# Optimization experiments

Measured on AMD Instinct MI355X. Metric: run time of the kernel, lower is better.

## Reference

```python
import jax, jax.numpy as jnp
import numpy as np
from jax import lax

N = 100000      # nodes
F_IN = 128      # dataset.num_features
H = 64          # hidden
E = 1600000     # edges
G = 1000        # graphs (equal-sized, contiguous)
PER = N // G    # nodes per graph = 100
K = 30          # sort-pool k
KS = 3          # conv1d kernel = num_layers


def setup_inputs() -> dict:
    key = jax.random.key(0)
    ks = jax.random.split(key, 20)
    lin = lambda k, i, o: (jax.random.normal(k, (i, o), jnp.float32) / np.sqrt(i)).astype(jnp.float32)
    return {
        "x": jax.random.normal(ks[0], (N, F_IN), jnp.float32),
        "src": jax.random.randint(ks[1], (E,), 0, N, dtype=jnp.int32),
        "dst": jax.random.randint(ks[2], (E,), 0, N, dtype=jnp.int32),
        "num_graphs": G,
        # SAGEConv 1: lin_l (aggr, with bias), lin_r (self, no bias)
        "wl1": lin(ks[3], F_IN, H), "wr1": lin(ks[4], F_IN, H), "b1": jnp.zeros((H,), jnp.float32),
        "wl2": lin(ks[5], H, H), "wr2": lin(ks[6], H, H), "b2": jnp.zeros((H,), jnp.float32),
        "wl3": lin(ks[7], H, H), "wr3": lin(ks[8], H, H), "b3": jnp.zeros((H,), jnp.float32),
        # Conv1d(hidden=64 -> 32, kernel=3): weight [O, I, K]
        "cw": (jax.random.normal(ks[9], (32, H, KS), jnp.float32) / np.sqrt(H * KS)).astype(jnp.float32),
        "cb": jnp.zeros((32,), jnp.float32),
        "w1": lin(ks[10], 32 * (K - KS + 1), H), "bb1": jnp.zeros((H,), jnp.float32),
        "w2": lin(ks[11], H, 1), "bb2": jnp.zeros((1,), jnp.float32),
    }


def _sage(x, src, dst, wl, wr, b, n):
    # PyG SAGEConv (mean aggr): lin_l(mean_{j->i} x_j) + lin_r(x_i)
    msum = jax.ops.segment_sum(x[src], dst, num_segments=n)           # [N, F]
    cnt = jax.ops.segment_sum(jnp.ones((src.shape[0],), x.dtype), dst, num_segments=n)
    mean = msum / jnp.maximum(cnt, 1.0)[:, None]
    return mean @ wl + b + x @ wr


def reference(x, src, dst, num_graphs, wl1, wr1, b1, wl2, wr2, b2, wl3, wr3, b3, cw, cb, w1, bb1, w2, bb2):
    n = x.shape[0]
    h = jax.nn.relu(_sage(x, src, dst, wl1, wr1, b1, n))
    h = jax.nn.relu(_sage(h, src, dst, wl2, wr2, b2, n))
    h = jax.nn.relu(_sage(h, src, dst, wl3, wr3, b3, n))
    # SortAggregation(k): per-graph, sort nodes by last feature channel (desc), keep top-k.
    # batch = contiguous equal-sized graphs -> dense reshape is exact.
    hg = h.reshape(num_graphs, PER, H)                                # [G, PER, H]
    order = jnp.argsort(-hg[:, :, -1], axis=1)[:, :K]                 # [G, K]
    topk = jnp.take_along_axis(hg, order[:, :, None], axis=1)         # [G, K, H]
    xc = jnp.transpose(topk, (0, 2, 1))                               # [G, H, K]
    y = lax.conv_general_dilated(xc, cw, (1,), 'VALID',
                                 dimension_numbers=('NCH', 'OIH', 'NCH'))
    y = jax.nn.relu(y + cb[None, :, None])                            # [G, 32, K-KS+1]
    y = y.reshape(num_graphs, -1)
    y = jax.nn.relu(y @ w1 + bb1)
    # dropout: eval mode -> identity
    return y @ w2 + bb2                                               # [G, 1]
```

## Files before the change

kernel.cpp:

```cpp
#include <hip/hip_runtime.h>

#define NN 100000
#define EE 1600000
#define GG 1000
#define PERG 100
#define KK 30
#define HH 64

#define NB 782
#define CAP 4096
#define CHB 4096
#define BUCKET_BLOCKS ((EE + CHB - 1) / CHB)
#define PROJ_BLOCKS ((NN + 127) / 128)

__device__ __forceinline__ void bucket_body(int bid, float* smem,
                                            const int* __restrict__ src,
                                            const int* __restrict__ dst,
                                            int* __restrict__ gcur,
                                            int* __restrict__ pairs) {
  int* lhist = (int*)smem;
  int* lbase = lhist + NB;
  int* lcur = lbase + NB;
  const int t = threadIdx.x;
  const int c0 = bid * CHB;
  const int c1 = min(c0 + CHB, EE);
  for (int b = t; b < NB; b += 256) {
    lhist[b] = 0;
    lcur[b] = 0;
  }
  __syncthreads();
  for (int e = c0 + t; e < c1; e += 256) atomicAdd(&lhist[dst[e] >> 7], 1);
  __syncthreads();
  for (int b = t; b < NB; b += 256) {
    int c = lhist[b];
    lbase[b] = c ? atomicAdd(&gcur[b], c) : 0;
  }
  __syncthreads();
  for (int e = c0 + t; e < c1; e += 256) {
    int d = dst[e];
    int b = d >> 7;
    int p = atomicAdd(&lcur[b], 1);
    pairs[b * CAP + lbase[b] + p] = (src[e] << 7) | (d & 127);
  }
}

template <int K>
__device__ __forceinline__ void proj_body(int bid, float* smem,
                                          const float* __restrict__ X,
                                          const float* __restrict__ WL,
                                          const float* __restrict__ WR,
                                          float* __restrict__ P,
                                          float* __restrict__ R) {
  constexpr int BM = 128, BK = 32, XSP = 40, WSP = 144;
  float* xs = smem;
  float* ws = smem + BM * XSP;
  const int t = threadIdx.x;
  const int row0 = bid * BM;
  const int tc = t & 15, tr = t >> 4;
  const int wcol = tc * 8 + (tc >> 2) * 4;

  float acc[8][8];
#pragma unroll
  for (int i = 0; i < 8; ++i)
#pragma unroll
    for (int j = 0; j < 8; ++j) acc[i][j] = 0.f;

  for (int k0 = 0; k0 < K; k0 += BK) {
    __syncthreads();
    for (int idx = t; idx < BM * 8; idx += 256) {
      int r = idx >> 3, c = idx & 7;
      int row = row0 + r;
      float4 v = make_float4(0.f, 0.f, 0.f, 0.f);
      if (row < NN) v = *reinterpret_cast<const float4*>(&X[(size_t)row * K + k0 + c * 4]);
      *reinterpret_cast<float4*>(&xs[r * XSP + c * 4]) = v;
    }
    for (int idx = t; idx < BK * 16; idx += 256) {
      int kr = idx >> 4, c4 = idx & 15;
      int gcl = c4 >> 1;
      int off = gcl * 8 + (gcl >> 2) * 4 + (c4 & 1) * 4;
      *reinterpret_cast<float4*>(&ws[kr * WSP + off]) =
          *reinterpret_cast<const float4*>(&WL[(k0 + kr) * 64 + c4 * 4]);
      int g2 = gcl + 8;
      int off2 = g2 * 8 + (g2 >> 2) * 4 + (c4 & 1) * 4;
      *reinterpret_cast<float4*>(&ws[kr * WSP + off2]) =
          *reinterpret_cast<const float4*>(&WR[(k0 + kr) * 64 + c4 * 4]);
    }
    __syncthreads();
    for (int kk4 = 0; kk4 < BK; kk4 += 4) {
      float4 a[8];
#pragma unroll
      for (int i = 0; i < 8; ++i)
        a[i] = *reinterpret_cast<const float4*>(&xs[(tr + 16 * i) * XSP + kk4]);
#pragma unroll
      for (int kk = 0; kk < 4; ++kk) {
        float4 b0 = *reinterpret_cast<const float4*>(&ws[(kk4 + kk) * WSP + wcol]);
        float4 b1 = *reinterpret_cast<const float4*>(&ws[(kk4 + kk) * WSP + wcol + 4]);
        float bv[8] = {b0.x, b0.y, b0.z, b0.w, b1.x, b1.y, b1.z, b1.w};
#pragma unroll
        for (int i = 0; i < 8; ++i) {
          float av = (kk == 0) ? a[i].x : (kk == 1) ? a[i].y : (kk == 2) ? a[i].z : a[i].w;
#pragma unroll
          for (int j = 0; j < 8; ++j) acc[i][j] = fmaf(av, bv[j], acc[i][j]);
        }
      }
    }
  }

  float* OUT = (tc < 8) ? P : R;
  int cb = (tc & 7) * 8;
#pragma unroll
  for (int i = 0; i < 8; ++i) {
    int row = row0 + tr + 16 * i;
    if (row < NN) {
      *reinterpret_cast<float4*>(&OUT[(size_t)row * 64 + cb]) =
          make_float4(acc[i][0], acc[i][1], acc[i][2], acc[i][3]);
      *reinterpret_cast<float4*>(&OUT[(size_t)row * 64 + cb + 4]) =
          make_float4(acc[i][4], acc[i][5], acc[i][6], acc[i][7]);
    }
  }
}

__global__ __launch_bounds__(256) void fused_bucket_proj(const int* __restrict__ src,
                                                         const int* __restrict__ dst,
                                                         int* __restrict__ gcur,
                                                         int* __restrict__ pairs,
                                                         const float* __restrict__ X,
                                                         const float* __restrict__ WL,
                                                         const float* __restrict__ WR,
                                                         float* __restrict__ P,
                                                         float* __restrict__ R) {
  __shared__ float smem[128 * 40 + 32 * 144];
  if (blockIdx.x < PROJ_BLOCKS)
    proj_body<128>(blockIdx.x, smem, X, WL, WR, P, R);
  else
    bucket_body(blockIdx.x - PROJ_BLOCKS, smem, src, dst, gcur, pairs);
}

template <int K>
__global__ __launch_bounds__(256) void proj_kernel(const float* __restrict__ X,
                                                   const float* __restrict__ WL,
                                                   const float* __restrict__ WR,
                                                   float* __restrict__ P,
                                                   float* __restrict__ R) {
  __shared__ float smem[128 * 40 + 32 * 144];
  proj_body<K>(blockIdx.x, smem, X, WL, WR, P, R);
}

__global__ __launch_bounds__(256) void csr_kernel(const int* __restrict__ gcur,
                                                  const int* __restrict__ pairs,
                                                  int* __restrict__ row_start,
                                                  int* __restrict__ cnt,
                                                  int* __restrict__ eidx) {
  __shared__ int vals[CAP];
  __shared__ int hist[128];
  __shared__ int offs[128];
  __shared__ int cur[128];
  __shared__ int red[4];
  const int b = blockIdx.x;
  const int t = threadIdx.x;
  int s = 0;
  for (int i = t; i < b; i += 256) s += gcur[i];
#pragma unroll
  for (int off = 32; off > 0; off >>= 1) s += __shfl_xor(s, off);
  if ((t & 63) == 0) red[t >> 6] = s;
  if (t < 128) {
    hist[t] = 0;
    cur[t] = 0;
  }
  __syncthreads();
  const int base = red[0] + red[1] + red[2] + red[3];
  const int nb = gcur[b];
  for (int i = t; i < nb; i += 256) {
    int v = pairs[b * CAP + i];
    vals[i] = v;
    atomicAdd(&hist[v & 127], 1);
  }
  __syncthreads();
  if (t < 128) {
    int ss = 0;
    for (int m = 0; m < t; ++m) ss += hist[m];
    offs[t] = ss;
    int node = b * 128 + t;
    if (node < NN) {
      row_start[node] = base + ss;
      cnt[node] = hist[t];
    }
  }
  __syncthreads();
  for (int i = t; i < nb; i += 256) {
    int v = vals[i];
    int ld = v & 127;
    int p = atomicAdd(&cur[ld], 1);
    eidx[base + offs[ld] + p] = v >> 7;
  }
}

__global__ __launch_bounds__(256) void agg_kernel(const float* __restrict__ P,
                                                  const float* __restrict__ R,
                                                  const float* __restrict__ bias,
                                                  const int* __restrict__ row_start,
                                                  const int* __restrict__ cnt,
                                                  const int* __restrict__ eidx,
                                                  float* __restrict__ h,
                                                  float* __restrict__ keys) {
  const int wv = (blockIdx.x * 256 + threadIdx.x) >> 6;
  const int lane = threadIdx.x & 63;
  const int q = lane >> 4;
  const int ql = lane & 15;
  const int node = wv * 4 + q;
  if (node >= NN) return;
  const int base = row_start[node];
  const int deg = cnt[node];
  float4 acc = make_float4(0.f, 0.f, 0.f, 0.f);

  for (int e0 = 0; e0 < deg; e0 += 16) {
    const int rem = deg - e0;
    const int ii = (ql < rem) ? ql : (rem - 1);
    int idx = eidx[base + e0 + ii];
#pragma unroll
    for (int j = 0; j < 16; ++j) {
      const int sj = __shfl(idx, (lane & 48) | j);
      const float wj = (j < rem) ? 1.f : 0.f;
      const float4 vj = *reinterpret_cast<const float4*>(&P[(size_t)sj * 64 + ql * 4]);
      acc.x = fmaf(wj, vj.x, acc.x);
      acc.y = fmaf(wj, vj.y, acc.y);
      acc.z = fmaf(wj, vj.z, acc.z);
      acc.w = fmaf(wj, vj.w, acc.w);
    }
  }

  const float dv = fmaxf((float)deg, 1.0f);
  float4 r4 = *reinterpret_cast<const float4*>(&R[(size_t)node * 64 + ql * 4]);
  float4 b4 = *reinterpret_cast<const float4*>(&bias[ql * 4]);
  float4 o;
  o.x = fmaxf(acc.x / dv + b4.x + r4.x, 0.f);
  o.y = fmaxf(acc.y / dv + b4.y + r4.y, 0.f);
  o.z = fmaxf(acc.z / dv + b4.z + r4.z, 0.f);
  o.w = fmaxf(acc.w / dv + b4.w + r4.w, 0.f);
  *reinterpret_cast<float4*>(&h[(size_t)node * 64 + ql * 4]) = o;
  if (keys != nullptr && ql == 15) keys[node] = o.w;
}

__global__ __launch_bounds__(256) void head_kernel(const float* __restrict__ h,
                                                   const float* __restrict__ keysArr,
                                                   const float* __restrict__ cw,
                                                   const float* __restrict__ cb,
                                                   const float* __restrict__ w1,
                                                   const float* __restrict__ bb1,
                                                   const float* __restrict__ w2,
                                                   const float* __restrict__ bb2,
                                                   float* __restrict__ out) {
  __shared__ float key[PERG];
  __shared__ int sel[KK];
  __shared__ float feat[34 * 65];
  __shared__ float cwT[192 * 33];
  __shared__ float z[896];
  __shared__ float psum[256];
  const int g = blockIdx.x;
  const int t = threadIdx.x;

  for (int idx = t; idx < 32 * 192; idx += 256) {
    int o = idx / 192, k = idx % 192;
    cwT[k * 33 + o] = cw[idx];
  }
  if (t < PERG) key[t] = keysArr[g * PERG + t];
  __syncthreads();

  if (t < PERG) {
    float kv = key[t];
    int r = 0;
    for (int m = 0; m < PERG; ++m) {
      float km = key[m];
      r += (int)((km > kv) || (km == kv && m < t));
    }
    if (r < KK) sel[r] = t;
  }
  __syncthreads();

  for (int idx = t; idx < KK * HH; idx += 256) {
    int r = idx >> 6, f = idx & 63;
    feat[r * 65 + f] = h[(size_t)(g * PERG + sel[r]) * HH + f];
  }
  __syncthreads();

  {
    const int o = t & 31;
    const int pg = t >> 5;
    float zacc[4] = {0.f, 0.f, 0.f, 0.f};
    int i = 0, tt = 0;
    for (int k = 0; k < 192; ++k) {
      float c = cwT[k * 33 + o];
#pragma unroll
      for (int j = 0; j < 4; ++j) {
        int p = pg + 8 * j;
        zacc[j] = fmaf(c, feat[(p + tt) * 65 + i], zacc[j]);
      }
      if (++tt == 3) {
        tt = 0;
        ++i;
      }
    }
    float cbo = cb[o];
#pragma unroll
    for (int j = 0; j < 4; ++j) {
      int p = pg + 8 * j;
      if (p < 28) z[o * 28 + p] = fmaxf(zacc[j] + cbo, 0.f);
    }
  }
  __syncthreads();

  {
    const int hh = t & 63;
    const int quarter = t >> 6;
    const int q0 = quarter * 224;
    float acc = 0.f;
    for (int q = 0; q < 224; ++q)
      acc = fmaf(z[q0 + q], w1[(size_t)(q0 + q) * 64 + hh], acc);
    psum[t] = acc;
  }
  __syncthreads();

  if (t < 64) {
    float o1 = fmaxf(bb1[t] + psum[t] + psum[t + 64] + psum[t + 128] + psum[t + 192], 0.f);
    float v = o1 * w2[t];
#pragma unroll
    for (int off = 32; off > 0; off >>= 1) v += __shfl_down(v, off);
    if (t == 0) out[g] = v + bb2[0];
  }
}

extern "C" void kernel_launch(void* const* d_in, const int* in_sizes, int n_in,
                              void* d_out, int out_size, void* d_ws, size_t ws_size,
                              hipStream_t stream) {
  const float* x = (const float*)d_in[0];
  const int* src = (const int*)d_in[1];
  const int* dst = (const int*)d_in[2];
  const float* wl1 = (const float*)d_in[4];
  const float* wr1 = (const float*)d_in[5];
  const float* b1 = (const float*)d_in[6];
  const float* wl2 = (const float*)d_in[7];
  const float* wr2 = (const float*)d_in[8];
  const float* b2 = (const float*)d_in[9];
  const float* wl3 = (const float*)d_in[10];
  const float* wr3 = (const float*)d_in[11];
  const float* b3 = (const float*)d_in[12];
  const float* cw = (const float*)d_in[13];
  const float* cb = (const float*)d_in[14];
  const float* w1 = (const float*)d_in[15];
  const float* bb1 = (const float*)d_in[16];
  const float* w2 = (const float*)d_in[17];
  const float* bb2 = (const float*)d_in[18];
  float* out = (float*)d_out;

  char* w = (char*)d_ws;
  auto carve = [&](size_t bytes) {
    char* p = w;
    w += (bytes + 255) & ~(size_t)255;
    return p;
  };
  int* row_start = (int*)carve((size_t)NN * 4);
  int* cnt = (int*)carve((size_t)NN * 4);
  int* eidx = (int*)carve((size_t)EE * 4);
  float* P = (float*)carve((size_t)NN * 64 * 4);
  float* R = (float*)carve((size_t)NN * 64 * 4);
  float* hbuf = (float*)carve((size_t)NN * 64 * 4);
  float* keys = (float*)carve((size_t)NN * 4);
  int* gcur = (int*)carve((size_t)NB * 4);
  int* pairs = (int*)hbuf;

  hipMemsetAsync(gcur, 0, (size_t)NB * 4, stream);
  fused_bucket_proj<<<BUCKET_BLOCKS + PROJ_BLOCKS, 256, 0, stream>>>(
      src, dst, gcur, pairs, x, wl1, wr1, P, R);
  csr_kernel<<<NB, 256, 0, stream>>>(gcur, pairs, row_start, cnt, eidx);

  const int aggGrid = (NN + 15) / 16;
  agg_kernel<<<aggGrid, 256, 0, stream>>>(P, R, b1, row_start, cnt, eidx, hbuf, nullptr);
  proj_kernel<64><<<PROJ_BLOCKS, 256, 0, stream>>>(hbuf, wl2, wr2, P, R);
  agg_kernel<<<aggGrid, 256, 0, stream>>>(P, R, b2, row_start, cnt, eidx, hbuf, nullptr);
  proj_kernel<64><<<PROJ_BLOCKS, 256, 0, stream>>>(hbuf, wl3, wr3, P, R);
  agg_kernel<<<aggGrid, 256, 0, stream>>>(P, R, b3, row_start, cnt, eidx, hbuf, keys);
  head_kernel<<<GG, 256, 0, stream>>>(hbuf, keys, cw, cb, w1, bb1, w2, bb2, out);
}
```

Before: 497.0 us.

## Fuse mean-aggregation with next layer's projection into one layer kernel

```diff
diff --git a/kernel.cpp b/kernel.cpp
--- a/kernel.cpp
+++ b/kernel.cpp
@@ -12,6 +12,7 @@
 #define CHB 4096
 #define BUCKET_BLOCKS ((EE + CHB - 1) / CHB)
 #define PROJ_BLOCKS ((NN + 127) / 128)
+#define LAYER_BLOCKS PROJ_BLOCKS
 
 __device__ __forceinline__ void bucket_body(int bid, float* smem,
                                             const int* __restrict__ src,
@@ -239,6 +240,101 @@
   o.w = fmaxf(acc.w / dv + b4.w + r4.w, 0.f);
   *reinterpret_cast<float4*>(&h[(size_t)node * 64 + ql * 4]) = o;
   if (keys != nullptr && ql == 15) keys[node] = o.w;
+}
+
+__global__ __launch_bounds__(256) void layer_kernel(const float* __restrict__ P,
+                                                    const float* __restrict__ R,
+                                                    const float* __restrict__ bias,
+                                                    const int* __restrict__ row_start,
+                                                    const int* __restrict__ cnt,
+                                                    const int* __restrict__ eidx,
+                                                    const float* __restrict__ WL,
+                                                    const float* __restrict__ WR,
+                                                    float* __restrict__ Pout,
+                                                    float* __restrict__ Rout) {
+  __shared__ float hs[128 * 68];
+  const int t = threadIdx.x;
+  const int lane = t & 63;
+  const int qd = t >> 4;
+  const int ql = t & 15;
+  const int row0 = blockIdx.x * 128;
+
+  for (int p = 0; p < 8; ++p) {
+    const int r = qd + 16 * p;
+    const int node = row0 + r;
+    float4 acc = make_float4(0.f, 0.f, 0.f, 0.f);
+    int deg = 0;
+    if (node < NN) {
+      const int base = row_start[node];
+      deg = cnt[node];
+      for (int e0 = 0; e0 < deg; e0 += 16) {
+        const int rem = deg - e0;
+        const int ii = (ql < rem) ? ql : (rem - 1);
+        int idx = eidx[base + e0 + ii];
+#pragma unroll
+        for (int j = 0; j < 16; ++j) {
+          const int sj = __shfl(idx, (lane & 48) | j);
+          const float wj = (j < rem) ? 1.f : 0.f;
+          const float4 vj = *reinterpret_cast<const float4*>(&P[(size_t)sj * 64 + ql * 4]);
+          acc.x = fmaf(wj, vj.x, acc.x);
+          acc.y = fmaf(wj, vj.y, acc.y);
+          acc.z = fmaf(wj, vj.z, acc.z);
+          acc.w = fmaf(wj, vj.w, acc.w);
+        }
+      }
+      const float dv = fmaxf((float)deg, 1.0f);
+      float4 r4 = *reinterpret_cast<const float4*>(&R[(size_t)node * 64 + ql * 4]);
+      float4 b4 = *reinterpret_cast<const float4*>(&bias[ql * 4]);
+      acc.x = fmaxf(acc.x / dv + b4.x + r4.x, 0.f);
+      acc.y = fmaxf(acc.y / dv + b4.y + r4.y, 0.f);
+      acc.z = fmaxf(acc.z / dv + b4.z + r4.z, 0.f);
+      acc.w = fmaxf(acc.w / dv + b4.w + r4.w, 0.f);
+    }
+    *reinterpret_cast<float4*>(&hs[r * 68 + ql * 4]) = acc;
+  }
+  __syncthreads();
+
+  const int tc = t & 15, tr = t >> 4;
+  const float* WB = (tc < 8) ? WL : WR;
+  const int wcolg = (tc & 7) * 8;
+
+  float acc[8][8];
+#pragma unroll
+  for (int i = 0; i < 8; ++i)
+#pragma unroll
+    for (int j = 0; j < 8; ++j) acc[i][j] = 0.f;
+
+  for (int kk4 = 0; kk4 < 64; kk4 += 4) {
+    float4 a[8];
+#pragma unroll
+    for (int i = 0; i < 8; ++i)
+      a[i] = *reinterpret_cast<const float4*>(&hs[(tr + 16 * i) * 68 + kk4]);
+#pragma unroll
+    for (int kk = 0; kk < 4; ++kk) {
+      float4 b0 = *reinterpret_cast<const float4*>(&WB[(kk4 + kk) * 64 + wcolg]);
+      float4 b1 = *reinterpret_cast<const float4*>(&WB[(kk4 + kk) * 64 + wcolg + 4]);
+      float bv[8] = {b0.x, b0.y, b0.z, b0.w, b1.x, b1.y, b1.z, b1.w};
+#pragma unroll
+      for (int i = 0; i < 8; ++i) {
+        float av = (kk == 0) ? a[i].x : (kk == 1) ? a[i].y : (kk == 2) ? a[i].z : a[i].w;
+#pragma unroll
+        for (int j = 0; j < 8; ++j) acc[i][j] = fmaf(av, bv[j], acc[i][j]);
+      }
+    }
+  }
+
+  float* OUT = (tc < 8) ? Pout : Rout;
+  const int cb = (tc & 7) * 8;
+#pragma unroll
+  for (int i = 0; i < 8; ++i) {
+    int row = row0 + tr + 16 * i;
+    if (row < NN) {
+      *reinterpret_cast<float4*>(&OUT[(size_t)row * 64 + cb]) =
+          make_float4(acc[i][0], acc[i][1], acc[i][2], acc[i][3]);
+      *reinterpret_cast<float4*>(&OUT[(size_t)row * 64 + cb + 4]) =
+          make_float4(acc[i][4], acc[i][5], acc[i][6], acc[i][7]);
+    }
+  }
 }
 
 __global__ __launch_bounds__(256) void head_kernel(const float* __restrict__ h,
@@ -353,9 +449,12 @@
   float* out = (float*)d_out;
 
   char* w = (char*)d_ws;
+  size_t used = 0;
   auto carve = [&](size_t bytes) {
     char* p = w;
-    w += (bytes + 255) & ~(size_t)255;
+    size_t pad = (bytes + 255) & ~(size_t)255;
+    w += pad;
+    used += pad;
     return p;
   };
   int* row_start = (int*)carve((size_t)NN * 4);
@@ -366,7 +465,12 @@
   float* hbuf = (float*)carve((size_t)NN * 64 * 4);
   float* keys = (float*)carve((size_t)NN * 4);
   int* gcur = (int*)carve((size_t)NB * 4);
+  size_t used_base = used;
+  float* R2 = (float*)carve((size_t)NN * 64 * 4);
   int* pairs = (int*)hbuf;
+  float* P2 = hbuf;
+
+  const bool fused_layers = (used <= ws_size);
 
   hipMemsetAsync(gcur, 0, (size_t)NB * 4, stream);
   fused_bucket_proj<<<BUCKET_BLOCKS + PROJ_BLOCKS, 256, 0, stream>>>(
@@ -374,10 +478,19 @@
   csr_kernel<<<NB, 256, 0, stream>>>(gcur, pairs, row_start, cnt, eidx);
 
   const int aggGrid = (NN + 15) / 16;
-  agg_kernel<<<aggGrid, 256, 0, stream>>>(P, R, b1, row_start, cnt, eidx, hbuf, nullptr);
-  proj_kernel<64><<<PROJ_BLOCKS, 256, 0, stream>>>(hbuf, wl2, wr2, P, R);
-  agg_kernel<<<aggGrid, 256, 0, stream>>>(P, R, b2, row_start, cnt, eidx, hbuf, nullptr);
-  proj_kernel<64><<<PROJ_BLOCKS, 256, 0, stream>>>(hbuf, wl3, wr3, P, R);
-  agg_kernel<<<aggGrid, 256, 0, stream>>>(P, R, b3, row_start, cnt, eidx, hbuf, keys);
+  if (fused_layers) {
+    layer_kernel<<<LAYER_BLOCKS, 256, 0, stream>>>(P, R, b1, row_start, cnt, eidx,
+                                                   wl2, wr2, P2, R2);
+    layer_kernel<<<LAYER_BLOCKS, 256, 0, stream>>>(P2, R2, b2, row_start, cnt, eidx,
+                                                   wl3, wr3, P, R);
+    agg_kernel<<<aggGrid, 256, 0, stream>>>(P, R, b3, row_start, cnt, eidx, hbuf, keys);
+  } else {
+    (void)used_base;
+    agg_kernel<<<aggGrid, 256, 0, stream>>>(P, R, b1, row_start, cnt, eidx, hbuf, nullptr);
+    proj_kernel<64><<<PROJ_BLOCKS, 256, 0, stream>>>(hbuf, wl2, wr2, P, R);
+    agg_kernel<<<aggGrid, 256, 0, stream>>>(P, R, b2, row_start, cnt, eidx, hbuf, nullptr);
+    proj_kernel<64><<<PROJ_BLOCKS, 256, 0, stream>>>(hbuf, wl3, wr3, P, R);
+    agg_kernel<<<aggGrid, 256, 0, stream>>>(P, R, b3, row_start, cnt, eidx, hbuf, keys);
+  }
   head_kernel<<<GG, 256, 0, stream>>>(hbuf, keys, cw, cb, w1, bb1, w2, bb2, out);
 }
```

Result: no change. 490.7 us (-1.3%).
